# Kernel optimization log

Measured on AMD Instinct MI355X. Metric: run time of the kernel, lower is better.

## Reference

```python
import jax, jax.numpy as jnp
import numpy as np

N, E, F_IN, HEADS, OUT_PER_HEAD = 50000, 1600000, 128, 4, 32
NEG_SLOPE = 0.2  # LeakyReLU slope used by standard GATConv


def setup_inputs() -> dict:
    key = jax.random.key(0)
    ks = jax.random.split(key, 7)
    x = jax.random.normal(ks[0], (N, F_IN), dtype=jnp.float32)
    edge_src = jax.random.randint(ks[1], (E,), 0, N, dtype=jnp.int64)
    edge_dst = jax.random.randint(ks[2], (E,), 0, N, dtype=jnp.int64)
    W = jax.random.normal(ks[3], (F_IN, HEADS * OUT_PER_HEAD), dtype=jnp.float32) / np.float32(np.sqrt(F_IN))
    a_src = jax.random.normal(ks[4], (HEADS, OUT_PER_HEAD), dtype=jnp.float32) * 0.1
    a_dst = jax.random.normal(ks[5], (HEADS, OUT_PER_HEAD), dtype=jnp.float32) * 0.1
    bias = jnp.zeros((HEADS * OUT_PER_HEAD,), dtype=jnp.float32)
    return {"x": x, "W": W, "a_src": a_src, "a_dst": a_dst, "bias": bias,
            "edge_src": edge_src, "edge_dst": edge_dst}


def reference(x, W, a_src, a_dst, bias, edge_src, edge_dst):
    # GATConv with concat=True over a static edge list (the faithful
    # static-shape form of tf.where(adj>0.5) -> gather -> GAT -> scatter).
    n = x.shape[0]
    H, D = a_src.shape
    h = (x @ W).reshape(n, H, D)                      # [N,H,D] projected features
    # per-node attention logits for source / destination roles
    e_s = jnp.einsum('nhd,hd->nh', h, a_src)          # [N,H]
    e_d = jnp.einsum('nhd,hd->nh', h, a_dst)          # [N,H]
    # per-edge logits with LeakyReLU
    e = jax.nn.leaky_relu(e_s[edge_src] + e_d[edge_dst], NEG_SLOPE)  # [E,H]
    # numerically stable softmax over incoming edges of each destination node
    m = jax.ops.segment_max(e, edge_dst, num_segments=n)             # [N,H]
    m = jnp.where(jnp.isfinite(m), m, 0.0)
    alpha = jnp.exp(e - m[edge_dst])                                 # [E,H]
    denom = jax.ops.segment_sum(alpha, edge_dst, num_segments=n)     # [N,H]
    alpha = alpha / jnp.where(denom > 0, denom, 1.0)[edge_dst]
    # weighted aggregation of source features onto destinations
    msgs = alpha[:, :, None] * h[edge_src]                           # [E,H,D]
    out = jax.ops.segment_sum(msgs, edge_dst, num_segments=n)        # [N,H,D]
    return out.reshape(n, H * D) + bias
```

## Files before the change

kernel.cpp:

```cpp
#include <hip/hip_runtime.h>
#include <math.h>

#define NEG_SLOPE 0.2f
#define NB1 256
#define SCAN_CHUNK 1024
#define XROW 136

typedef __attribute__((ext_vector_type(8))) short short8;
typedef __attribute__((ext_vector_type(4))) float floatx4;

__device__ __forceinline__ unsigned short f2bf(float f) {
    unsigned int u = __float_as_uint(f);
    u += 0x7fffu + ((u >> 16) & 1u);
    return (unsigned short)(u >> 16);
}
__device__ __forceinline__ float bf2f(unsigned short b) {
    return __uint_as_float(((unsigned int)b) << 16);
}

__global__ __launch_bounds__(256) void prep_w_kernel(
    const float* __restrict__ W, unsigned short* __restrict__ WThi,
    unsigned short* __restrict__ WTlo)
{
    const int idx = blockIdx.x * 256 + threadIdx.x;
    const int j = idx >> 7, k = idx & 127;
    const float w = W[k * 128 + j];
    const unsigned short hi = f2bf(w);
    const unsigned short lo = f2bf(w - bf2f(hi));
    WThi[idx] = hi;
    WTlo[idx] = lo;
}

__global__ __launch_bounds__(256) void mfma_gemm_kernel(
    const float* __restrict__ x, const unsigned short* __restrict__ WThi,
    const unsigned short* __restrict__ WTlo, unsigned short* __restrict__ hb,
    int n)
{
    __shared__ unsigned short Xhi[32 * XROW];
    __shared__ unsigned short Xlo[32 * XROW];
    const int t = threadIdx.x;
    const int wv = t >> 6, lane = t & 63;
    const int l16 = lane & 15, quad = lane >> 4;
    const int node_base = blockIdx.x * 32;

    short8 bh[4][2], bl[4][2];
    #pragma unroll
    for (int c = 0; c < 4; ++c) {
        #pragma unroll
        for (int u = 0; u < 2; ++u) {
            const int j = (wv * 2 + u) * 16 + l16;
            const int ko = c * 32 + quad * 8;
            bh[c][u] = *(const short8*)&WThi[j * 128 + ko];
            bl[c][u] = *(const short8*)&WTlo[j * 128 + ko];
        }
    }

    for (int i = t; i < 1024; i += 256) {
        const int nd = i >> 5;
        const int k4 = i & 31;
        float4 xv = make_float4(0.f, 0.f, 0.f, 0.f);
        if (node_base + nd < n)
            xv = ((const float4*)(x + (size_t)(node_base + nd) * 128))[k4];
        const unsigned short h0 = f2bf(xv.x), h1 = f2bf(xv.y),
                             h2 = f2bf(xv.z), h3 = f2bf(xv.w);
        const unsigned short l0 = f2bf(xv.x - bf2f(h0)), l1 = f2bf(xv.y - bf2f(h1)),
                             l2 = f2bf(xv.z - bf2f(h2)), l3 = f2bf(xv.w - bf2f(h3));
        *(ushort4*)&Xhi[nd * XROW + k4 * 4] = make_ushort4(h0, h1, h2, h3);
        *(ushort4*)&Xlo[nd * XROW + k4 * 4] = make_ushort4(l0, l1, l2, l3);
    }
    __syncthreads();

    floatx4 acc[2][2] = {};
    #pragma unroll
    for (int c = 0; c < 4; ++c) {
        const int ko = c * 32 + quad * 8;
        short8 ah[2], al[2];
        #pragma unroll
        for (int r = 0; r < 2; ++r) {
            ah[r] = *(const short8*)&Xhi[(r * 16 + l16) * XROW + ko];
            al[r] = *(const short8*)&Xlo[(r * 16 + l16) * XROW + ko];
        }
        #pragma unroll
        for (int r = 0; r < 2; ++r)
        #pragma unroll
        for (int u = 0; u < 2; ++u) {
            acc[r][u] = __builtin_amdgcn_mfma_f32_16x16x32_bf16(ah[r], bl[c][u], acc[r][u], 0, 0, 0);
            acc[r][u] = __builtin_amdgcn_mfma_f32_16x16x32_bf16(al[r], bh[c][u], acc[r][u], 0, 0, 0);
            acc[r][u] = __builtin_amdgcn_mfma_f32_16x16x32_bf16(ah[r], bh[c][u], acc[r][u], 0, 0, 0);
        }
    }

    #pragma unroll
    for (int r = 0; r < 2; ++r)
    #pragma unroll
    for (int u = 0; u < 2; ++u) {
        const int feat = (wv * 2 + u) * 16 + l16;
        #pragma unroll
        for (int g = 0; g < 4; ++g) {
            const int node = node_base + r * 16 + quad * 4 + g;
            if (node < n)
                hb[(size_t)node * 128 + feat] = f2bf(acc[r][u][g]);
        }
    }
}

__global__ __launch_bounds__(256) void esed_kernel(
    const unsigned short* __restrict__ hb, const float* __restrict__ a_src,
    const float* __restrict__ a_dst, float* __restrict__ es,
    float* __restrict__ ed, int n)
{
    const int lane = threadIdx.x & 63;
    const int wv = threadIdx.x >> 6;
    const int node = blockIdx.x * 4 + wv;
    if (node >= n) return;
    const unsigned int u = *(const unsigned int*)&hb[(size_t)node * 128 + lane * 2];
    const float f0 = __uint_as_float(u << 16);
    const float f1 = __uint_as_float(u & 0xffff0000u);
    const float2 av = *(const float2*)(a_src + lane * 2);
    const float2 bv = *(const float2*)(a_dst + lane * 2);
    float ps = f0 * av.x + f1 * av.y;
    float pd = f0 * bv.x + f1 * bv.y;
    #pragma unroll
    for (int o = 8; o >= 1; o >>= 1) {
        ps += __shfl_xor(ps, o);
        pd += __shfl_xor(pd, o);
    }
    if ((lane & 15) == 0) {
        es[node * 4 + (lane >> 4)] = ps;
        ed[node * 4 + (lane >> 4)] = pd;
    }
}

__global__ __launch_bounds__(256) void p1_bucket_hist(
    const int* __restrict__ dst, int* __restrict__ counts_mat,
    int e, int nbuck)
{
    __shared__ int cnt[256];
    const int t = threadIdx.x;
    cnt[t] = 0;
    __syncthreads();
    const int per = (e + NB1 - 1) / NB1;
    const int lo = blockIdx.x * per;
    const int hi = min(e, lo + per);
    for (int i = lo + t; i < hi; i += 256)
        atomicAdd(&cnt[dst[i] >> 8], 1);
    __syncthreads();
    for (int b = t; b < nbuck; b += 256)
        counts_mat[b * NB1 + blockIdx.x] = cnt[b];
}

__device__ __forceinline__ int wave_incl_scan(int v, int lane) {
    #pragma unroll
    for (int o = 1; o < 64; o <<= 1) {
        const int t = __shfl_up(v, o);
        if (lane >= o) v += t;
    }
    return v;
}

__global__ __launch_bounds__(256) void scanA_kernel(
    const int* __restrict__ in, int* __restrict__ bsum, int m)
{
    __shared__ int ws[4];
    const int t = threadIdx.x;
    const int lane = t & 63;
    const int wv = t >> 6;
    const int idx = blockIdx.x * SCAN_CHUNK + t * 4;
    int4 v = {0, 0, 0, 0};
    if (idx + 3 < m) v = *(const int4*)(in + idx);
    else {
        if (idx + 0 < m) v.x = in[idx + 0];
        if (idx + 1 < m) v.y = in[idx + 1];
        if (idx + 2 < m) v.z = in[idx + 2];
        if (idx + 3 < m) v.w = in[idx + 3];
    }
    const int s = v.x + v.y + v.z + v.w;
    const int incl = wave_incl_scan(s, lane);
    if (lane == 63) ws[wv] = incl;
    __syncthreads();
    if (t == 0) bsum[blockIdx.x] = ws[0] + ws[1] + ws[2] + ws[3];
}

__global__ __launch_bounds__(64) void scanB_kernel(
    const int* __restrict__ bsum, int* __restrict__ ebsum, int nb)
{
    const int lane = threadIdx.x;
    const int v = (lane < nb) ? bsum[lane] : 0;
    const int incl = wave_incl_scan(v, lane);
    if (lane < nb) ebsum[lane] = incl - v;
}

__global__ __launch_bounds__(256) void scanC_kernel(
    const int* __restrict__ in, const int* __restrict__ ebsum,
    int* __restrict__ outx, int m)
{
    __shared__ int ws[4];
    const int t = threadIdx.x;
    const int lane = t & 63;
    const int wv = t >> 6;
    const int idx = blockIdx.x * SCAN_CHUNK + t * 4;
    int4 v = {0, 0, 0, 0};
    if (idx + 3 < m) v = *(const int4*)(in + idx);
    else {
        if (idx + 0 < m) v.x = in[idx + 0];
        if (idx + 1 < m) v.y = in[idx + 1];
        if (idx + 2 < m) v.z = in[idx + 2];
        if (idx + 3 < m) v.w = in[idx + 3];
    }
    const int s = v.x + v.y + v.z + v.w;
    const int incl = wave_incl_scan(s, lane);
    if (lane == 63) ws[wv] = incl;
    __syncthreads();
    int wpre = 0;
    #pragma unroll
    for (int w = 0; w < 4; ++w) if (w < wv) wpre += ws[w];
    int p = ebsum[blockIdx.x] + wpre + (incl - s);
    if (idx + 0 < m) outx[idx + 0] = p; p += v.x;
    if (idx + 1 < m) outx[idx + 1] = p; p += v.y;
    if (idx + 2 < m) outx[idx + 2] = p; p += v.z;
    if (idx + 3 < m) outx[idx + 3] = p;
}

__global__ __launch_bounds__(256) void p3_bucket_scatter(
    const int* __restrict__ src, const int* __restrict__ dst,
    const int* __restrict__ base_mat, int* __restrict__ ebuf,
    int e, int nbuck)
{
    __shared__ int cur[256];
    const int t = threadIdx.x;
    if (t < nbuck) cur[t] = base_mat[t * NB1 + blockIdx.x];
    __syncthreads();
    const int per = (e + NB1 - 1) / NB1;
    const int lo = blockIdx.x * per;
    const int hi = min(e, lo + per);
    for (int i = lo + t; i < hi; i += 256) {
        const int d = dst[i];
        const int pos = atomicAdd(&cur[d >> 8], 1);
        ebuf[pos] = src[i] | ((d & 0xFF) << 16);
    }
}

__global__ __launch_bounds__(256) void p4_bucket_sort(
    const int* __restrict__ ebuf, const int* __restrict__ base_mat,
    int* __restrict__ offsets, int* __restrict__ count,
    int* __restrict__ sorted_src, int e, int n, int nbuck)
{
    __shared__ int hcnt[256], hexcl[256], cur[256];
    const int b = blockIdx.x;
    const int t = threadIdx.x;
    const int lane = t & 63;
    const int wv = t >> 6;
    const int start = base_mat[b * NB1];
    const int end = (b + 1 < nbuck) ? base_mat[(b + 1) * NB1] : e;
    hcnt[t] = 0;
    __syncthreads();
    for (int i = start + t; i < end; i += 256)
        atomicAdd(&hcnt[(ebuf[i] >> 16) & 0xFF], 1);
    __syncthreads();
    if (wv == 0) {
        const int i0 = lane * 4;
        const int c0 = hcnt[i0], c1 = hcnt[i0 + 1], c2 = hcnt[i0 + 2], c3 = hcnt[i0 + 3];
        const int s = c0 + c1 + c2 + c3;
        const int incl = wave_incl_scan(s, lane);
        int ex = incl - s;
        hexcl[i0] = ex; ex += c0;
        hexcl[i0 + 1] = ex; ex += c1;
        hexcl[i0 + 2] = ex; ex += c2;
        hexcl[i0 + 3] = ex;
    }
    __syncthreads();
    {
        const int gd = b * 256 + t;
        const int o = start + hexcl[t];
        cur[t] = o;
        if (gd < n) { offsets[gd] = o; count[gd] = hcnt[t]; }
    }
    __syncthreads();
    for (int i = start + t; i < end; i += 256) {
        const int v = ebuf[i];
        const int pos = atomicAdd(&cur[(v >> 16) & 0xFF], 1);
        sorted_src[pos] = v & 0xFFFF;
    }
}

__global__ __launch_bounds__(256) void aggregate_kernel(
    const unsigned short* __restrict__ hb, const float* __restrict__ es,
    const float* __restrict__ ed, const float* __restrict__ bias,
    const int* __restrict__ offsets, const int* __restrict__ degree,
    const int* __restrict__ sorted_src, float* __restrict__ out, int n)
{
    const int lane = threadIdx.x & 63;
    const int wv = threadIdx.x >> 6;
    const int nwaves = gridDim.x * 4;
    const int l16 = lane & 15;
    const int quad = lane >> 4;
    const int f0 = l16 * 8;
    const int hh = l16 >> 2;

    for (int node = blockIdx.x * 4 + wv; node < n; node += nwaves) {
        const int off = offsets[node];
        const int deg = degree[node];
        const float edh = ed[(size_t)node * 4 + hh];

        float a0 = 0.f, a1 = 0.f, a2 = 0.f, a3 = 0.f;
        float a4 = 0.f, a5 = 0.f, a6 = 0.f, a7 = 0.f;
        float wsum = 0.f;
        for (int c0 = 0; c0 < deg; c0 += 64) {
            const int cnt = min(64, deg - c0);
            int s_l = 0;
            if (c0 + lane < deg) s_l = sorted_src[off + c0 + lane];
            const int groups = (cnt + 3) >> 2;
            for (int i = 0; i < groups; ++i) {
                const int ci = 4 * i + quad;
                const int s = __shfl(s_l, ci);
                if (ci < cnt) {
                    float lg = es[(size_t)s * 4 + hh] + edh;
                    lg = lg > 0.f ? lg : NEG_SLOPE * lg;
                    const float w = __expf(lg);
                    const uint4 hv = *(const uint4*)&hb[(size_t)s * 128 + f0];
                    a0 = fmaf(w, __uint_as_float(hv.x << 16),         a0);
                    a1 = fmaf(w, __uint_as_float(hv.x & 0xffff0000u), a1);
                    a2 = fmaf(w, __uint_as_float(hv.y << 16),         a2);
                    a3 = fmaf(w, __uint_as_float(hv.y & 0xffff0000u), a3);
                    a4 = fmaf(w, __uint_as_float(hv.z << 16),         a4);
                    a5 = fmaf(w, __uint_as_float(hv.z & 0xffff0000u), a5);
                    a6 = fmaf(w, __uint_as_float(hv.w << 16),         a6);
                    a7 = fmaf(w, __uint_as_float(hv.w & 0xffff0000u), a7);
                    wsum += w;
                }
            }
        }
        #pragma unroll
        for (int o = 16; o <= 32; o <<= 1) {
            a0 += __shfl_xor(a0, o); a1 += __shfl_xor(a1, o);
            a2 += __shfl_xor(a2, o); a3 += __shfl_xor(a3, o);
            a4 += __shfl_xor(a4, o); a5 += __shfl_xor(a5, o);
            a6 += __shfl_xor(a6, o); a7 += __shfl_xor(a7, o);
            wsum += __shfl_xor(wsum, o);
        }
        if (quad == 0) {
            const float inv = 1.f / ((wsum > 0.f) ? wsum : 1.f);
            const float4 b0 = *(const float4*)(bias + f0);
            const float4 b1 = *(const float4*)(bias + f0 + 4);
            float4 o0, o1;
            o0.x = a0 * inv + b0.x; o0.y = a1 * inv + b0.y;
            o0.z = a2 * inv + b0.z; o0.w = a3 * inv + b0.w;
            o1.x = a4 * inv + b1.x; o1.y = a5 * inv + b1.y;
            o1.z = a6 * inv + b1.z; o1.w = a7 * inv + b1.w;
            *(float4*)(out + (size_t)node * 128 + f0) = o0;
            *(float4*)(out + (size_t)node * 128 + f0 + 4) = o1;
        }
    }
}

extern "C" void kernel_launch(void* const* d_in, const int* in_sizes, int n_in,
                              void* d_out, int out_size, void* d_ws, size_t ws_size,
                              hipStream_t stream)
{
    const float* x      = (const float*)d_in[0];
    const float* W      = (const float*)d_in[1];
    const float* a_src  = (const float*)d_in[2];
    const float* a_dst  = (const float*)d_in[3];
    const float* bias   = (const float*)d_in[4];
    const int*   e_src  = (const int*)d_in[5];
    const int*   e_dst  = (const int*)d_in[6];
    float* out = (float*)d_out;

    const int n = in_sizes[0] / 128;
    const int e = in_sizes[5];
    const int nbuck = (n + 255) >> 8;
    const int m = nbuck * NB1;
    const int nchunks = (m + SCAN_CHUNK - 1) / SCAN_CHUNK;

    char* ws = (char*)d_ws;
    size_t o = 0;
    auto alloc = [&](size_t bytes) { void* p = ws + o; o += (bytes + 255) & ~(size_t)255; return p; };
    unsigned short* hb   = (unsigned short*)alloc((size_t)n * 128 * sizeof(unsigned short));
    unsigned short* WThi = (unsigned short*)alloc(128 * 128 * sizeof(unsigned short));
    unsigned short* WTlo = (unsigned short*)alloc(128 * 128 * sizeof(unsigned short));
    float* es      = (float*)alloc((size_t)n * 4 * sizeof(float));
    float* ed      = (float*)alloc((size_t)n * 4 * sizeof(float));
    int* counts_mat= (int*)alloc((size_t)m * sizeof(int));
    int* base_mat  = (int*)alloc((size_t)m * sizeof(int));
    int* offsets   = (int*)alloc((size_t)n * sizeof(int));
    int* count     = (int*)alloc((size_t)n * sizeof(int));
    int* bsum      = (int*)alloc(64 * sizeof(int));
    int* ebsum     = (int*)alloc(64 * sizeof(int));
    int* ebuf      = (int*)alloc((size_t)e * sizeof(int));
    int* sortedsrc = (int*)alloc((size_t)e * sizeof(int));
    (void)ws_size; (void)n_in; (void)out_size;

    prep_w_kernel<<<64, 256, 0, stream>>>(W, WThi, WTlo);
    mfma_gemm_kernel<<<(n + 31) / 32, 256, 0, stream>>>(x, WThi, WTlo, hb, n);
    esed_kernel<<<(n + 3) / 4, 256, 0, stream>>>(hb, a_src, a_dst, es, ed, n);
    p1_bucket_hist<<<NB1, 256, 0, stream>>>(e_dst, counts_mat, e, nbuck);
    scanA_kernel<<<nchunks, 256, 0, stream>>>(counts_mat, bsum, m);
    scanB_kernel<<<1, 64, 0, stream>>>(bsum, ebsum, nchunks);
    scanC_kernel<<<nchunks, 256, 0, stream>>>(counts_mat, ebsum, base_mat, m);
    p3_bucket_scatter<<<NB1, 256, 0, stream>>>(e_src, e_dst, base_mat, ebuf, e, nbuck);
    p4_bucket_sort<<<nbuck, 256, 0, stream>>>(ebuf, base_mat, offsets, count,
                                              sortedsrc, e, n, nbuck);
    aggregate_kernel<<<(n + 3) / 4, 256, 0, stream>>>(hb, es, ed, bias, offsets,
                                                      count, sortedsrc, out, n);
}
```

Baseline: 223.6 us.

## Fuse attention logits into GEMM, simplify bucket sort, widen aggregation per lane

Computes per-node source and destination attention logits inside the MFMA GEMM epilogue, which removes the separate esed kernel and its re-read of the bf16 features. The multi-kernel per-block histogram and three-stage scan is replaced by packed-edge counting with global atomics, a single small scan, and a scatter staged in shared memory. Each lane in the aggregation kernel now handles 16 features and two edges per iteration, putting more loads in flight. The cost is global atomics on bucket cursors, an extra packed edge buffer, and higher register pressure in aggregation.

```diff
diff --git a/kernel.cpp b/kernel.cpp
--- a/kernel.cpp
+++ b/kernel.cpp
@@ -3,7 +3,6 @@
 
 #define NEG_SLOPE 0.2f
 #define NB1 256
-#define SCAN_CHUNK 1024
 #define XROW 136
 
 typedef __attribute__((ext_vector_type(8))) short short8;
@@ -16,6 +15,23 @@
 }
 __device__ __forceinline__ float bf2f(unsigned short b) {
     return __uint_as_float(((unsigned int)b) << 16);
+}
+__device__ __forceinline__ float u2fl(unsigned int u) {
+    return __uint_as_float(u << 16);
+}
+__device__ __forceinline__ float u2fh(unsigned int u) {
+    return __uint_as_float(u & 0xffff0000u);
+}
+
+__device__ __forceinline__ void fma8(float* a, int o, float wt, const uint4& hv) {
+    a[o + 0] = fmaf(wt, u2fl(hv.x), a[o + 0]);
+    a[o + 1] = fmaf(wt, u2fh(hv.x), a[o + 1]);
+    a[o + 2] = fmaf(wt, u2fl(hv.y), a[o + 2]);
+    a[o + 3] = fmaf(wt, u2fh(hv.y), a[o + 3]);
+    a[o + 4] = fmaf(wt, u2fl(hv.z), a[o + 4]);
+    a[o + 5] = fmaf(wt, u2fh(hv.z), a[o + 5]);
+    a[o + 6] = fmaf(wt, u2fl(hv.w), a[o + 6]);
+    a[o + 7] = fmaf(wt, u2fh(hv.w), a[o + 7]);
 }
 
 __global__ __launch_bounds__(256) void prep_w_kernel(
@@ -33,8 +49,9 @@
 
 __global__ __launch_bounds__(256) void mfma_gemm_kernel(
     const float* __restrict__ x, const unsigned short* __restrict__ WThi,
-    const unsigned short* __restrict__ WTlo, unsigned short* __restrict__ hb,
-    int n)
+    const unsigned short* __restrict__ WTlo, const float* __restrict__ a_src,
+    const float* __restrict__ a_dst, unsigned short* __restrict__ hb,
+    float* __restrict__ es, float* __restrict__ ed, int n)
 {
     __shared__ unsigned short Xhi[32 * XROW];
     __shared__ unsigned short Xlo[32 * XROW];
@@ -90,168 +107,134 @@
         }
     }
 
-    #pragma unroll
-    for (int r = 0; r < 2; ++r)
+    float asv[2], adv[2];
     #pragma unroll
     for (int u = 0; u < 2; ++u) {
         const int feat = (wv * 2 + u) * 16 + l16;
+        asv[u] = a_src[feat];
+        adv[u] = a_dst[feat];
+    }
+    #pragma unroll
+    for (int r = 0; r < 2; ++r) {
+        #pragma unroll
+        for (int u = 0; u < 2; ++u) {
+            const int feat = (wv * 2 + u) * 16 + l16;
+            #pragma unroll
+            for (int g = 0; g < 4; ++g) {
+                const int node = node_base + r * 16 + quad * 4 + g;
+                if (node < n)
+                    hb[(size_t)node * 128 + feat] = f2bf(acc[r][u][g]);
+            }
+        }
         #pragma unroll
         for (int g = 0; g < 4; ++g) {
+            float ps = acc[r][0][g] * asv[0] + acc[r][1][g] * asv[1];
+            float pd = acc[r][0][g] * adv[0] + acc[r][1][g] * adv[1];
+            #pragma unroll
+            for (int o = 8; o >= 1; o >>= 1) {
+                ps += __shfl_xor(ps, o);
+                pd += __shfl_xor(pd, o);
+            }
             const int node = node_base + r * 16 + quad * 4 + g;
-            if (node < n)
-                hb[(size_t)node * 128 + feat] = f2bf(acc[r][u][g]);
-        }
-    }
-}
-
-__global__ __launch_bounds__(256) void esed_kernel(
-    const unsigned short* __restrict__ hb, const float* __restrict__ a_src,
-    const float* __restrict__ a_dst, float* __restrict__ es,
-    float* __restrict__ ed, int n)
-{
-    const int lane = threadIdx.x & 63;
-    const int wv = threadIdx.x >> 6;
-    const int node = blockIdx.x * 4 + wv;
-    if (node >= n) return;
-    const unsigned int u = *(const unsigned int*)&hb[(size_t)node * 128 + lane * 2];
-    const float f0 = __uint_as_float(u << 16);
-    const float f1 = __uint_as_float(u & 0xffff0000u);
-    const float2 av = *(const float2*)(a_src + lane * 2);
-    const float2 bv = *(const float2*)(a_dst + lane * 2);
-    float ps = f0 * av.x + f1 * av.y;
-    float pd = f0 * bv.x + f1 * bv.y;
-    #pragma unroll
-    for (int o = 8; o >= 1; o >>= 1) {
-        ps += __shfl_xor(ps, o);
-        pd += __shfl_xor(pd, o);
-    }
-    if ((lane & 15) == 0) {
-        es[node * 4 + (lane >> 4)] = ps;
-        ed[node * 4 + (lane >> 4)] = pd;
-    }
-}
-
-__global__ __launch_bounds__(256) void p1_bucket_hist(
-    const int* __restrict__ dst, int* __restrict__ counts_mat,
+            if (l16 == 0 && node < n) {
+                es[node * 4 + wv] = ps;
+                ed[node * 4 + wv] = pd;
+            }
+        }
+    }
+}
+
+__global__ __launch_bounds__(256) void b1_pack_count(
+    const int* __restrict__ src, const int* __restrict__ dst,
+    unsigned int* __restrict__ packed, int* __restrict__ btot,
     int e, int nbuck)
 {
     __shared__ int cnt[256];
     const int t = threadIdx.x;
     cnt[t] = 0;
-    __syncthreads();
-    const int per = (e + NB1 - 1) / NB1;
-    const int lo = blockIdx.x * per;
-    const int hi = min(e, lo + per);
-    for (int i = lo + t; i < hi; i += 256)
-        atomicAdd(&cnt[dst[i] >> 8], 1);
-    __syncthreads();
-    for (int b = t; b < nbuck; b += 256)
-        counts_mat[b * NB1 + blockIdx.x] = cnt[b];
-}
-
-__device__ __forceinline__ int wave_incl_scan(int v, int lane) {
-    #pragma unroll
-    for (int o = 1; o < 64; o <<= 1) {
-        const int t = __shfl_up(v, o);
-        if (lane >= o) v += t;
-    }
-    return v;
-}
-
-__global__ __launch_bounds__(256) void scanA_kernel(
-    const int* __restrict__ in, int* __restrict__ bsum, int m)
-{
-    __shared__ int ws[4];
-    const int t = threadIdx.x;
-    const int lane = t & 63;
-    const int wv = t >> 6;
-    const int idx = blockIdx.x * SCAN_CHUNK + t * 4;
-    int4 v = {0, 0, 0, 0};
-    if (idx + 3 < m) v = *(const int4*)(in + idx);
-    else {
-        if (idx + 0 < m) v.x = in[idx + 0];
-        if (idx + 1 < m) v.y = in[idx + 1];
-        if (idx + 2 < m) v.z = in[idx + 2];
-        if (idx + 3 < m) v.w = in[idx + 3];
-    }
-    const int s = v.x + v.y + v.z + v.w;
-    const int incl = wave_incl_scan(s, lane);
-    if (lane == 63) ws[wv] = incl;
-    __syncthreads();
-    if (t == 0) bsum[blockIdx.x] = ws[0] + ws[1] + ws[2] + ws[3];
-}
-
-__global__ __launch_bounds__(64) void scanB_kernel(
-    const int* __restrict__ bsum, int* __restrict__ ebsum, int nb)
-{
-    const int lane = threadIdx.x;
-    const int v = (lane < nb) ? bsum[lane] : 0;
-    const int incl = wave_incl_scan(v, lane);
-    if (lane < nb) ebsum[lane] = incl - v;
-}
-
-__global__ __launch_bounds__(256) void scanC_kernel(
-    const int* __restrict__ in, const int* __restrict__ ebsum,
-    int* __restrict__ outx, int m)
-{
-    __shared__ int ws[4];
-    const int t = threadIdx.x;
-    const int lane = t & 63;
-    const int wv = t >> 6;
-    const int idx = blockIdx.x * SCAN_CHUNK + t * 4;
-    int4 v = {0, 0, 0, 0};
-    if (idx + 3 < m) v = *(const int4*)(in + idx);
-    else {
-        if (idx + 0 < m) v.x = in[idx + 0];
-        if (idx + 1 < m) v.y = in[idx + 1];
-        if (idx + 2 < m) v.z = in[idx + 2];
-        if (idx + 3 < m) v.w = in[idx + 3];
-    }
-    const int s = v.x + v.y + v.z + v.w;
-    const int incl = wave_incl_scan(s, lane);
-    if (lane == 63) ws[wv] = incl;
-    __syncthreads();
-    int wpre = 0;
-    #pragma unroll
-    for (int w = 0; w < 4; ++w) if (w < wv) wpre += ws[w];
-    int p = ebsum[blockIdx.x] + wpre + (incl - s);
-    if (idx + 0 < m) outx[idx + 0] = p; p += v.x;
-    if (idx + 1 < m) outx[idx + 1] = p; p += v.y;
-    if (idx + 2 < m) outx[idx + 2] = p; p += v.z;
-    if (idx + 3 < m) outx[idx + 3] = p;
-}
-
-__global__ __launch_bounds__(256) void p3_bucket_scatter(
-    const int* __restrict__ src, const int* __restrict__ dst,
-    const int* __restrict__ base_mat, int* __restrict__ ebuf,
-    int e, int nbuck)
-{
-    __shared__ int cur[256];
-    const int t = threadIdx.x;
-    if (t < nbuck) cur[t] = base_mat[t * NB1 + blockIdx.x];
     __syncthreads();
     const int per = (e + NB1 - 1) / NB1;
     const int lo = blockIdx.x * per;
     const int hi = min(e, lo + per);
     for (int i = lo + t; i < hi; i += 256) {
         const int d = dst[i];
-        const int pos = atomicAdd(&cur[d >> 8], 1);
-        ebuf[pos] = src[i] | ((d & 0xFF) << 16);
+        atomicAdd(&cnt[d >> 8], 1);
+        packed[i] = (unsigned int)src[i] | ((unsigned int)(d & 0xFF) << 16)
+                  | ((unsigned int)(d >> 8) << 24);
+    }
+    __syncthreads();
+    if (t < nbuck && cnt[t] > 0) atomicAdd(&btot[t], cnt[t]);
+}
+
+__device__ __forceinline__ int wave_incl_scan(int v, int lane) {
+    #pragma unroll
+    for (int o = 1; o < 64; o <<= 1) {
+        const int t = __shfl_up(v, o);
+        if (lane >= o) v += t;
+    }
+    return v;
+}
+
+__global__ __launch_bounds__(256) void scan_small_kernel(
+    const int* __restrict__ btot, int* __restrict__ base,
+    int* __restrict__ gcursor, int nbuck, int e)
+{
+    __shared__ int ws[4];
+    const int t = threadIdx.x;
+    const int lane = t & 63;
+    const int wv = t >> 6;
+    const int v = (t < nbuck) ? btot[t] : 0;
+    const int incl = wave_incl_scan(v, lane);
+    if (lane == 63) ws[wv] = incl;
+    __syncthreads();
+    int wpre = 0;
+    #pragma unroll
+    for (int w = 0; w < 4; ++w) if (w < wv) wpre += ws[w];
+    const int excl = wpre + incl - v;
+    if (t < nbuck) { base[t] = excl; gcursor[t] = excl; }
+    if (t == 0) base[nbuck] = e;
+}
+
+__global__ __launch_bounds__(256) void b2_scatter(
+    const unsigned int* __restrict__ packed, int* __restrict__ gcursor,
+    int* __restrict__ ebuf, int e, int nbuck)
+{
+    __shared__ int cnt[256];
+    __shared__ int cur[256];
+    __shared__ unsigned int stash[6272];
+    const int t = threadIdx.x;
+    cnt[t] = 0;
+    __syncthreads();
+    const int per = (e + NB1 - 1) / NB1;
+    const int lo = blockIdx.x * per;
+    const int m = min(e, lo + per) - lo;
+    for (int j = t; j < m; j += 256) {
+        const unsigned int v = packed[lo + j];
+        stash[j] = v;
+        atomicAdd(&cnt[v >> 24], 1);
+    }
+    __syncthreads();
+    if (t < nbuck) cur[t] = (cnt[t] > 0) ? atomicAdd(&gcursor[t], cnt[t]) : 0;
+    __syncthreads();
+    for (int j = t; j < m; j += 256) {
+        const unsigned int v = stash[j];
+        const int pos = atomicAdd(&cur[v >> 24], 1);
+        ebuf[pos] = (int)(v & 0xFFFFFFu);
     }
 }
 
 __global__ __launch_bounds__(256) void p4_bucket_sort(
-    const int* __restrict__ ebuf, const int* __restrict__ base_mat,
+    const int* __restrict__ ebuf, const int* __restrict__ base,
     int* __restrict__ offsets, int* __restrict__ count,
-    int* __restrict__ sorted_src, int e, int n, int nbuck)
+    int* __restrict__ sorted_src, int n, int nbuck)
 {
     __shared__ int hcnt[256], hexcl[256], cur[256];
     const int b = blockIdx.x;
     const int t = threadIdx.x;
     const int lane = t & 63;
     const int wv = t >> 6;
-    const int start = base_mat[b * NB1];
-    const int end = (b + 1 < nbuck) ? base_mat[(b + 1) * NB1] : e;
+    const int start = base[b];
+    const int end = base[b + 1];
     hcnt[t] = 0;
     __syncthreads();
     for (int i = start + t; i < end; i += 256)
@@ -292,63 +275,64 @@
     const int lane = threadIdx.x & 63;
     const int wv = threadIdx.x >> 6;
     const int nwaves = gridDim.x * 4;
-    const int l16 = lane & 15;
-    const int quad = lane >> 4;
-    const int f0 = l16 * 8;
-    const int hh = l16 >> 2;
+    const int l8 = lane & 7;
+    const int oct = lane >> 3;
+    const int f0 = l8 * 16;
+    const int hh = l8 >> 1;
 
     for (int node = blockIdx.x * 4 + wv; node < n; node += nwaves) {
         const int off = offsets[node];
         const int deg = degree[node];
         const float edh = ed[(size_t)node * 4 + hh];
 
-        float a0 = 0.f, a1 = 0.f, a2 = 0.f, a3 = 0.f;
-        float a4 = 0.f, a5 = 0.f, a6 = 0.f, a7 = 0.f;
+        float a[16];
+        #pragma unroll
+        for (int k = 0; k < 16; ++k) a[k] = 0.f;
         float wsum = 0.f;
+
         for (int c0 = 0; c0 < deg; c0 += 64) {
             const int cnt = min(64, deg - c0);
             int s_l = 0;
             if (c0 + lane < deg) s_l = sorted_src[off + c0 + lane];
-            const int groups = (cnt + 3) >> 2;
-            for (int i = 0; i < groups; ++i) {
-                const int ci = 4 * i + quad;
-                const int s = __shfl(s_l, ci);
-                if (ci < cnt) {
-                    float lg = es[(size_t)s * 4 + hh] + edh;
-                    lg = lg > 0.f ? lg : NEG_SLOPE * lg;
-                    const float w = __expf(lg);
-                    const uint4 hv = *(const uint4*)&hb[(size_t)s * 128 + f0];
-                    a0 = fmaf(w, __uint_as_float(hv.x << 16),         a0);
-                    a1 = fmaf(w, __uint_as_float(hv.x & 0xffff0000u), a1);
-                    a2 = fmaf(w, __uint_as_float(hv.y << 16),         a2);
-                    a3 = fmaf(w, __uint_as_float(hv.y & 0xffff0000u), a3);
-                    a4 = fmaf(w, __uint_as_float(hv.z << 16),         a4);
-                    a5 = fmaf(w, __uint_as_float(hv.z & 0xffff0000u), a5);
-                    a6 = fmaf(w, __uint_as_float(hv.w << 16),         a6);
-                    a7 = fmaf(w, __uint_as_float(hv.w & 0xffff0000u), a7);
-                    wsum += w;
-                }
-            }
-        }
-        #pragma unroll
-        for (int o = 16; o <= 32; o <<= 1) {
-            a0 += __shfl_xor(a0, o); a1 += __shfl_xor(a1, o);
-            a2 += __shfl_xor(a2, o); a3 += __shfl_xor(a3, o);
-            a4 += __shfl_xor(a4, o); a5 += __shfl_xor(a5, o);
-            a6 += __shfl_xor(a6, o); a7 += __shfl_xor(a7, o);
+            const int groups = (cnt + 7) >> 3;
+            for (int i = 0; i < groups; i += 2) {
+                const int ci0 = 8 * i + oct;
+                const int ci1 = ci0 + 8;
+                const int s0 = __shfl(s_l, ci0);
+                const int s1 = __shfl(s_l, ci1);
+                const float e0 = es[(size_t)s0 * 4 + hh];
+                const float e1 = es[(size_t)s1 * 4 + hh];
+                const uint4 hA0 = *(const uint4*)&hb[(size_t)s0 * 128 + f0];
+                const uint4 hB0 = *(const uint4*)&hb[(size_t)s0 * 128 + f0 + 8];
+                const uint4 hA1 = *(const uint4*)&hb[(size_t)s1 * 128 + f0];
+                const uint4 hB1 = *(const uint4*)&hb[(size_t)s1 * 128 + f0 + 8];
+                float lg0 = e0 + edh; lg0 = lg0 > 0.f ? lg0 : NEG_SLOPE * lg0;
+                float lg1 = e1 + edh; lg1 = lg1 > 0.f ? lg1 : NEG_SLOPE * lg1;
+                const float w0 = (ci0 < cnt) ? __expf(lg0) : 0.f;
+                const float w1 = (ci1 < cnt) ? __expf(lg1) : 0.f;
+                fma8(a, 0, w0, hA0); fma8(a, 8, w0, hB0);
+                fma8(a, 0, w1, hA1); fma8(a, 8, w1, hB1);
+                wsum += w0 + w1;
+            }
+        }
+        #pragma unroll
+        for (int o = 8; o <= 32; o <<= 1) {
+            #pragma unroll
+            for (int k = 0; k < 16; ++k) a[k] += __shfl_xor(a[k], o);
             wsum += __shfl_xor(wsum, o);
         }
-        if (quad == 0) {
+        if (oct == 0) {
             const float inv = 1.f / ((wsum > 0.f) ? wsum : 1.f);
-            const float4 b0 = *(const float4*)(bias + f0);
-            const float4 b1 = *(const float4*)(bias + f0 + 4);
-            float4 o0, o1;
-            o0.x = a0 * inv + b0.x; o0.y = a1 * inv + b0.y;
-            o0.z = a2 * inv + b0.z; o0.w = a3 * inv + b0.w;
-            o1.x = a4 * inv + b1.x; o1.y = a5 * inv + b1.y;
-            o1.z = a6 * inv + b1.z; o1.w = a7 * inv + b1.w;
-            *(float4*)(out + (size_t)node * 128 + f0) = o0;
-            *(float4*)(out + (size_t)node * 128 + f0 + 4) = o1;
+            #pragma unroll
+            for (int q = 0; q < 4; ++q) {
+                const float4 bq = *(const float4*)(bias + f0 + q * 4);
+                float4 o4;
+                o4.x = a[q * 4 + 0] * inv + bq.x;
+                o4.y = a[q * 4 + 1] * inv + bq.y;
+                o4.z = a[q * 4 + 2] * inv + bq.z;
+                o4.w = a[q * 4 + 3] * inv + bq.w;
+                *(float4*)(out + (size_t)node * 128 + f0 + q * 4) = o4;
+            }
         }
     }
 }
@@ -369,8 +353,6 @@
     const int n = in_sizes[0] / 128;
     const int e = in_sizes[5];
     const int nbuck = (n + 255) >> 8;
-    const int m = nbuck * NB1;
-    const int nchunks = (m + SCAN_CHUNK - 1) / SCAN_CHUNK;
 
     char* ws = (char*)d_ws;
     size_t o = 0;
@@ -380,26 +362,26 @@
     unsigned short* WTlo = (unsigned short*)alloc(128 * 128 * sizeof(unsigned short));
     float* es      = (float*)alloc((size_t)n * 4 * sizeof(float));
     float* ed      = (float*)alloc((size_t)n * 4 * sizeof(float));
-    int* counts_mat= (int*)alloc((size_t)m * sizeof(int));
-    int* base_mat  = (int*)alloc((size_t)m * sizeof(int));
+    unsigned int* packed = (unsigned int*)alloc((size_t)e * sizeof(unsigned int));
+    int* ebuf      = (int*)alloc((size_t)e * sizeof(int));
+    int* sortedsrc = (int*)alloc((size_t)e * sizeof(int));
+    int* btot      = (int*)alloc((size_t)(nbuck) * sizeof(int));
+    int* base      = (int*)alloc((size_t)(nbuck + 1) * sizeof(int));
+    int* gcursor   = (int*)alloc((size_t)(nbuck) * sizeof(int));
     int* offsets   = (int*)alloc((size_t)n * sizeof(int));
     int* count     = (int*)alloc((size_t)n * sizeof(int));
-    int* bsum      = (int*)alloc(64 * sizeof(int));
-    int* ebsum     = (int*)alloc(64 * sizeof(int));
-    int* ebuf      = (int*)alloc((size_t)e * sizeof(int));
-    int* sortedsrc = (int*)alloc((size_t)e * sizeof(int));
     (void)ws_size; (void)n_in; (void)out_size;
 
+    (void)hipMemsetAsync(btot, 0, (size_t)nbuck * sizeof(int), stream);
+
     prep_w_kernel<<<64, 256, 0, stream>>>(W, WThi, WTlo);
-    mfma_gemm_kernel<<<(n + 31) / 32, 256, 0, stream>>>(x, WThi, WTlo, hb, n);
-    esed_kernel<<<(n + 3) / 4, 256, 0, stream>>>(hb, a_src, a_dst, es, ed, n);
-    p1_bucket_hist<<<NB1, 256, 0, stream>>>(e_dst, counts_mat, e, nbuck);
-    scanA_kernel<<<nchunks, 256, 0, stream>>>(counts_mat, bsum, m);
-    scanB_kernel<<<1, 64, 0, stream>>>(bsum, ebsum, nchunks);
-    scanC_kernel<<<nchunks, 256, 0, stream>>>(counts_mat, ebsum, base_mat, m);
-    p3_bucket_scatter<<<NB1, 256, 0, stream>>>(e_src, e_dst, base_mat, ebuf, e, nbuck);
-    p4_bucket_sort<<<nbuck, 256, 0, stream>>>(ebuf, base_mat, offsets, count,
-                                              sortedsrc, e, n, nbuck);
+    mfma_gemm_kernel<<<(n + 31) / 32, 256, 0, stream>>>(x, WThi, WTlo, a_src, a_dst,
+                                                        hb, es, ed, n);
+    b1_pack_count<<<NB1, 256, 0, stream>>>(e_src, e_dst, packed, btot, e, nbuck);
+    scan_small_kernel<<<1, 256, 0, stream>>>(btot, base, gcursor, nbuck, e);
+    b2_scatter<<<NB1, 256, 0, stream>>>(packed, gcursor, ebuf, e, nbuck);
+    p4_bucket_sort<<<nbuck, 256, 0, stream>>>(ebuf, base, offsets, count,
+                                              sortedsrc, n, nbuck);
     aggregate_kernel<<<(n + 3) / 4, 256, 0, stream>>>(hb, es, ed, bias, offsets,
                                                       count, sortedsrc, out, n);
 }
```

Result: no change. 226.8 us (+1.4%).
